# Kernel optimization log

Measured on AMD Instinct MI355X. Metric: run time of the kernel, lower is better.

The kernel has to match this reference:

```python
import jax, jax.numpy as jnp
import numpy as np

TEMPERATURE = 8.0  # sqrt(d_k) with d_k = 64
EPS = 1e-8


def setup_inputs() -> dict:
    key = jax.random.key(0)
    kq, kk, kv, km = jax.random.split(key, 4)
    B, L, D = 16, 2048, 64
    q = jax.random.normal(kq, (B, L, D), dtype=jnp.float32)
    k = jax.random.normal(kk, (B, L, D), dtype=jnp.float32)
    v = jax.random.normal(kv, (B, L, D), dtype=jnp.float32)
    # True entries are zeroed out AFTER softmax (post-softmax masking)
    mask = jax.random.randint(km, (B, L, L), 0, 2).astype(jnp.bool_)
    return {"q": q, "k": k, "v": v, "mask": mask}


def reference(q, k, v, mask):
    # attn scores: [B, Lq, Lk]
    attn = jnp.einsum("bqd,bkd->bqk", q, k) / TEMPERATURE
    attn = jax.nn.softmax(attn, axis=2)
    # post-softmax masking followed by renormalization (breaks flash-attn fusion)
    attn = jnp.where(mask, 0.0, attn)
    attn = attn / (jnp.sum(attn, axis=2, keepdims=True) + EPS)
    # dropout is identity in eval/reference mode
    output = jnp.einsum("bqk,bkd->bqd", attn, v)
    return output, attn
```

## Files before the change

### kernel.cpp

```cpp
#include <hip/hip_runtime.h>

#define BATCH 16
#define LSEQ 2048
#define DIM 64
#define TQ 16
#define SSTRIDE 2056
#define EPSV 1e-8f

typedef float f4 __attribute__((ext_vector_type(4)));
typedef _Float16 h4 __attribute__((ext_vector_type(4)));
typedef _Float16 h8 __attribute__((ext_vector_type(8)));
typedef int i4t __attribute__((ext_vector_type(4)));

__device__ inline h8 cvt_h8(f4 a, f4 b) {
    h8 r;
    r[0] = (_Float16)a[0]; r[1] = (_Float16)a[1];
    r[2] = (_Float16)a[2]; r[3] = (_Float16)a[3];
    r[4] = (_Float16)b[0]; r[5] = (_Float16)b[1];
    r[6] = (_Float16)b[2]; r[7] = (_Float16)b[3];
    return r;
}

__global__ __launch_bounds__(256)
void cvt_k_kernel(const float* __restrict__ k, _Float16* __restrict__ kh) {
    const int idx = blockIdx.x * 256 + threadIdx.x;
    f4 v = ((const f4*)k)[idx];
    h4 h;
    #pragma unroll
    for (int e = 0; e < 4; ++e) h[e] = (_Float16)v[e];
    ((h4*)kh)[idx] = h;
}

__global__ __launch_bounds__(256)
void tr_v_kernel(const float* __restrict__ v, _Float16* __restrict__ vt) {
    __shared__ float tile[64][65];
    const int b = blockIdx.y, k0 = blockIdx.x * 64, t = threadIdx.x;
    const float* vb = v + ((size_t)b * LSEQ + k0) * DIM;
    #pragma unroll
    for (int p = 0; p < 4; ++p) {
        const int row = p * 16 + (t >> 4), c4 = (t & 15) * 4;
        f4 val = *(const f4*)(vb + row * DIM + c4);
        #pragma unroll
        for (int e = 0; e < 4; ++e) tile[row][c4 + e] = val[e];
    }
    __syncthreads();
    _Float16* vtb = vt + (size_t)b * DIM * LSEQ;
    #pragma unroll
    for (int p = 0; p < 4; ++p) {
        const int d = p * 16 + (t >> 4), k4 = (t & 15) * 4;
        h4 h;
        #pragma unroll
        for (int e = 0; e < 4; ++e) h[e] = (_Float16)tile[k4 + e][d];
        *(h4*)(vtb + (size_t)d * LSEQ + k0 + k4) = h;
    }
}

__global__ __launch_bounds__(512, 4)
void attn_kernel(const float* __restrict__ q, const _Float16* __restrict__ kh,
                 const _Float16* __restrict__ vt, const int* __restrict__ mask,
                 float* __restrict__ out, float* __restrict__ attn)
{
    __shared__ __align__(16) _Float16 s_p[TQ][SSTRIDE];
    __shared__ float oacc[8][TQ * 16];
    __shared__ float s_inv[TQ];

    const int b    = blockIdx.y;
    const int q0   = blockIdx.x * TQ;
    const int tid  = threadIdx.x;
    const int w    = tid >> 6;
    const int lane = tid & 63;
    const int quad = lane >> 4;
    const int m16  = lane & 15;

    const float* qrow = q + ((size_t)b * LSEQ + q0 + m16) * DIM + quad * 8;
    h8 aq0 = cvt_h8(*(const f4*)(qrow),      *(const f4*)(qrow + 4));
    h8 aq1 = cvt_h8(*(const f4*)(qrow + 32), *(const f4*)(qrow + 36));

    for (int t = w; t < LSEQ / 16; t += 8) {
        const int c = t * 16;
        const _Float16* krow = kh + ((size_t)b * LSEQ + c + m16) * DIM + quad * 8;
        h8 bk0 = *(const h8*)(krow);
        h8 bk1 = *(const h8*)(krow + 32);
        f4 acc = {0.f, 0.f, 0.f, 0.f};
        acc = __builtin_amdgcn_mfma_f32_16x16x32_f16(aq0, bk0, acc, 0, 0, 0);
        acc = __builtin_amdgcn_mfma_f32_16x16x32_f16(aq1, bk1, acc, 0, 0, 0);
        #pragma unroll
        for (int r = 0; r < 4; ++r)
            s_p[quad * 4 + r][c + m16] = (_Float16)(acc[r] * 0.125f);
    }
    __syncthreads();

    #pragma unroll
    for (int rr = 0; rr < 2; ++rr) {
        const int row = 2 * w + rr;
        const int* mrow = mask + ((size_t)b * LSEQ + q0 + row) * LSEQ;

        i4t mv[8];
        #pragma unroll
        for (int j = 0; j < 8; ++j)
            mv[j] = __builtin_nontemporal_load((const i4t*)(mrow + lane * 4 + 256 * j));

        float sa = 0.f, sk = 0.f;
        h4 pk[8];
        #pragma unroll
        for (int j = 0; j < 8; ++j) {
            h4 hv = *(const h4*)(&s_p[row][lane * 4 + 256 * j]);
            #pragma unroll
            for (int e = 0; e < 4; ++e) {
                float p = __expf((float)hv[e]);
                sa += p;
                float pm = mv[j][e] ? 0.f : p;
                sk += pm;
                pk[j][e] = (_Float16)pm;
            }
        }
        #pragma unroll
        for (int off = 32; off >= 1; off >>= 1) {
            sa += __shfl_xor(sa, off);
            sk += __shfl_xor(sk, off);
        }
        const float inv_d = 1.f / (sk + EPSV * sa);
        if (lane == 0) s_inv[row] = inv_d;

        float* arow = attn + ((size_t)b * LSEQ + q0 + row) * LSEQ;
        #pragma unroll
        for (int j = 0; j < 8; ++j) {
            const int c = lane * 4 + 256 * j;
            *(h4*)(&s_p[row][c]) = pk[j];
            f4 pv;
            #pragma unroll
            for (int e = 0; e < 4; ++e) pv[e] = inv_d * (float)pk[j][e];
            __builtin_nontemporal_store(pv, (f4*)(&arow[c]));
        }
    }
    __syncthreads();

    {
        const int dt = w >> 1;
        const int kh_ = w & 1;
        const _Float16* vtr = vt + ((size_t)b * DIM + dt * 16 + m16) * LSEQ;
        f4 acc = {0.f, 0.f, 0.f, 0.f};
        for (int kb0 = kh_ * 1024; kb0 < kh_ * 1024 + 1024; kb0 += 32) {
            const int kk = kb0 + quad * 8;
            h8 af = *(const h8*)(&s_p[m16][kk]);
            h8 bf = *(const h8*)(vtr + kk);
            acc = __builtin_amdgcn_mfma_f32_16x16x32_f16(af, bf, acc, 0, 0, 0);
        }
        #pragma unroll
        for (int r = 0; r < 4; ++r)
            oacc[w][(quad * 4 + r) * 16 + m16] = acc[r];
    }
    __syncthreads();

    float* ob = out + ((size_t)b * LSEQ + q0) * DIM;
    #pragma unroll
    for (int it = 0; it < 2; ++it) {
        const int idx = tid + it * 512;
        const int row = idx >> 6;
        const int d   = idx & 63;
        const int dt2 = d >> 4, dc = d & 15;
        ob[row * DIM + d] = s_inv[row] *
            (oacc[2 * dt2][row * 16 + dc] + oacc[2 * dt2 + 1][row * 16 + dc]);
    }
}

__global__ __launch_bounds__(512, 4)
void attn_kernel_fb(const float* __restrict__ q, const float* __restrict__ k,
                    const float* __restrict__ v, const int* __restrict__ mask,
                    float* __restrict__ out, float* __restrict__ attn)
{
    __shared__ __align__(16) _Float16 s_p[TQ][SSTRIDE];
    __shared__ float oacc[8][TQ * 16];
    __shared__ float s_inv[TQ];

    const int b = blockIdx.y, q0 = blockIdx.x * TQ, tid = threadIdx.x;
    const int w = tid >> 6, lane = tid & 63, quad = lane >> 4, m16 = lane & 15;
    const float* kp = k + (size_t)b * LSEQ * DIM;
    const float* vp = v + (size_t)b * LSEQ * DIM;
    const float* qrow = q + ((size_t)b * LSEQ + q0 + m16) * DIM + quad * 8;
    h8 aq0 = cvt_h8(*(const f4*)(qrow),      *(const f4*)(qrow + 4));
    h8 aq1 = cvt_h8(*(const f4*)(qrow + 32), *(const f4*)(qrow + 36));

    for (int t = w; t < LSEQ / 16; t += 8) {
        const int c = t * 16;
        const float* krow = kp + (size_t)(c + m16) * DIM + quad * 8;
        h8 bk0 = cvt_h8(*(const f4*)(krow),      *(const f4*)(krow + 4));
        h8 bk1 = cvt_h8(*(const f4*)(krow + 32), *(const f4*)(krow + 36));
        f4 acc = {0.f, 0.f, 0.f, 0.f};
        acc = __builtin_amdgcn_mfma_f32_16x16x32_f16(aq0, bk0, acc, 0, 0, 0);
        acc = __builtin_amdgcn_mfma_f32_16x16x32_f16(aq1, bk1, acc, 0, 0, 0);
        #pragma unroll
        for (int r = 0; r < 4; ++r)
            s_p[quad * 4 + r][c + m16] = (_Float16)(acc[r] * 0.125f);
    }
    __syncthreads();

    #pragma unroll
    for (int rr = 0; rr < 2; ++rr) {
        const int row = 2 * w + rr;
        const int* mrow = mask + ((size_t)b * LSEQ + q0 + row) * LSEQ;
        i4t mv[8];
        #pragma unroll
        for (int j = 0; j < 8; ++j)
            mv[j] = __builtin_nontemporal_load((const i4t*)(mrow + lane * 4 + 256 * j));
        float sa = 0.f, sk = 0.f;
        h4 pk[8];
        #pragma unroll
        for (int j = 0; j < 8; ++j) {
            h4 hv = *(const h4*)(&s_p[row][lane * 4 + 256 * j]);
            #pragma unroll
            for (int e = 0; e < 4; ++e) {
                float p = __expf((float)hv[e]);
                sa += p;
                float pm = mv[j][e] ? 0.f : p;
                sk += pm;
                pk[j][e] = (_Float16)pm;
            }
        }
        #pragma unroll
        for (int off = 32; off >= 1; off >>= 1) {
            sa += __shfl_xor(sa, off);
            sk += __shfl_xor(sk, off);
        }
        const float inv_d = 1.f / (sk + EPSV * sa);
        if (lane == 0) s_inv[row] = inv_d;
        float* arow = attn + ((size_t)b * LSEQ + q0 + row) * LSEQ;
        #pragma unroll
        for (int j = 0; j < 8; ++j) {
            const int c = lane * 4 + 256 * j;
            *(h4*)(&s_p[row][c]) = pk[j];
            f4 pv;
            #pragma unroll
            for (int e = 0; e < 4; ++e) pv[e] = inv_d * (float)pk[j][e];
            __builtin_nontemporal_store(pv, (f4*)(&arow[c]));
        }
    }
    __syncthreads();

    {
        const int dt = w >> 1, kh_ = w & 1;
        f4 acc = {0.f, 0.f, 0.f, 0.f};
        for (int kb0 = kh_ * 1024; kb0 < kh_ * 1024 + 1024; kb0 += 32) {
            const int kk = kb0 + quad * 8;
            h8 af = *(const h8*)(&s_p[m16][kk]);
            const float* vcol = vp + (size_t)kk * DIM + dt * 16 + m16;
            h8 bf;
            #pragma unroll
            for (int j = 0; j < 8; ++j) bf[j] = (_Float16)vcol[j * DIM];
            acc = __builtin_amdgcn_mfma_f32_16x16x32_f16(af, bf, acc, 0, 0, 0);
        }
        #pragma unroll
        for (int r = 0; r < 4; ++r)
            oacc[w][(quad * 4 + r) * 16 + m16] = acc[r];
    }
    __syncthreads();

    float* ob = out + ((size_t)b * LSEQ + q0) * DIM;
    #pragma unroll
    for (int it = 0; it < 2; ++it) {
        const int idx = tid + it * 512;
        const int row = idx >> 6, d = idx & 63;
        const int dt2 = d >> 4, dc = d & 15;
        ob[row * DIM + d] = s_inv[row] *
            (oacc[2 * dt2][row * 16 + dc] + oacc[2 * dt2 + 1][row * 16 + dc]);
    }
}

extern "C" void kernel_launch(void* const* d_in, const int* in_sizes, int n_in,
                              void* d_out, int out_size, void* d_ws, size_t ws_size,
                              hipStream_t stream) {
    const float* q = (const float*)d_in[0];
    const float* k = (const float*)d_in[1];
    const float* v = (const float*)d_in[2];
    const int* mask = (const int*)d_in[3];
    float* out = (float*)d_out;
    float* attn = out + (size_t)BATCH * LSEQ * DIM;
    dim3 grid(LSEQ / TQ, BATCH);

    const size_t kv_elems = (size_t)BATCH * LSEQ * DIM;
    if (ws_size >= kv_elems * 2 * sizeof(_Float16)) {
        _Float16* kh = (_Float16*)d_ws;
        _Float16* vt = kh + kv_elems;
        cvt_k_kernel<<<kv_elems / 4 / 256, 256, 0, stream>>>(k, kh);
        tr_v_kernel<<<dim3(LSEQ / 64, BATCH), 256, 0, stream>>>(v, vt);
        attn_kernel<<<grid, 512, 0, stream>>>(q, kh, vt, mask, out, attn);
    } else {
        attn_kernel_fb<<<grid, 512, 0, stream>>>(q, k, v, mask, out, attn);
    }
}
```

Baseline: 539.7 us.

## Double query tile to 32 rows with 1024-thread blocks and prefetch mask

The attention kernel now processes 32 query rows per block with 16 waves, so each K and V fragment load feeds two MFMAs (rows A and B). This halves K/V global traffic per output. The first mask row is prefetched before the QK^T phase to overlap its latency, and exp is folded into exp2 with a pre-multiplied log2e scale. The cost is double the LDS use for scores (about 130KB per block), which limits occupancy to one block per CU, plus extra syncs in the output reduction.

```diff
diff --git a/kernel.cpp b/kernel.cpp
--- a/kernel.cpp
+++ b/kernel.cpp
@@ -3,9 +3,10 @@
 #define BATCH 16
 #define LSEQ 2048
 #define DIM 64
-#define TQ 16
+#define TQ 32
 #define SSTRIDE 2056
 #define EPSV 1e-8f
+#define SCALE_LOG2E 0.18033688011112042f
 
 typedef float f4 __attribute__((ext_vector_type(4)));
 typedef _Float16 h4 __attribute__((ext_vector_type(4)));
@@ -55,13 +56,13 @@
     }
 }
 
-__global__ __launch_bounds__(512, 4)
+__global__ __launch_bounds__(1024, 4)
 void attn_kernel(const float* __restrict__ q, const _Float16* __restrict__ kh,
                  const _Float16* __restrict__ vt, const int* __restrict__ mask,
                  float* __restrict__ out, float* __restrict__ attn)
 {
     __shared__ __align__(16) _Float16 s_p[TQ][SSTRIDE];
-    __shared__ float oacc[8][TQ * 16];
+    __shared__ float oacc[16][256];
     __shared__ float s_inv[TQ];
 
     const int b    = blockIdx.y;
@@ -72,44 +73,58 @@
     const int quad = lane >> 4;
     const int m16  = lane & 15;
 
-    const float* qrow = q + ((size_t)b * LSEQ + q0 + m16) * DIM + quad * 8;
-    h8 aq0 = cvt_h8(*(const f4*)(qrow),      *(const f4*)(qrow + 4));
-    h8 aq1 = cvt_h8(*(const f4*)(qrow + 32), *(const f4*)(qrow + 36));
-
-    for (int t = w; t < LSEQ / 16; t += 8) {
+    const int row0 = 2 * w;
+    const int* mrow0 = mask + ((size_t)b * LSEQ + q0 + row0) * LSEQ;
+    i4t mv0[8];
+    #pragma unroll
+    for (int j = 0; j < 8; ++j)
+        mv0[j] = __builtin_nontemporal_load((const i4t*)(mrow0 + lane * 4 + 256 * j));
+
+    const float* qrowA = q + ((size_t)b * LSEQ + q0 + m16) * DIM + quad * 8;
+    const float* qrowB = qrowA + 16 * DIM;
+    h8 aqA0 = cvt_h8(*(const f4*)(qrowA),      *(const f4*)(qrowA + 4));
+    h8 aqA1 = cvt_h8(*(const f4*)(qrowA + 32), *(const f4*)(qrowA + 36));
+    h8 aqB0 = cvt_h8(*(const f4*)(qrowB),      *(const f4*)(qrowB + 4));
+    h8 aqB1 = cvt_h8(*(const f4*)(qrowB + 32), *(const f4*)(qrowB + 36));
+
+    for (int t = w; t < LSEQ / 16; t += 16) {
         const int c = t * 16;
         const _Float16* krow = kh + ((size_t)b * LSEQ + c + m16) * DIM + quad * 8;
         h8 bk0 = *(const h8*)(krow);
         h8 bk1 = *(const h8*)(krow + 32);
-        f4 acc = {0.f, 0.f, 0.f, 0.f};
-        acc = __builtin_amdgcn_mfma_f32_16x16x32_f16(aq0, bk0, acc, 0, 0, 0);
-        acc = __builtin_amdgcn_mfma_f32_16x16x32_f16(aq1, bk1, acc, 0, 0, 0);
-        #pragma unroll
-        for (int r = 0; r < 4; ++r)
-            s_p[quad * 4 + r][c + m16] = (_Float16)(acc[r] * 0.125f);
-    }
-    __syncthreads();
+        f4 accA = {0.f, 0.f, 0.f, 0.f}, accB = {0.f, 0.f, 0.f, 0.f};
+        accA = __builtin_amdgcn_mfma_f32_16x16x32_f16(aqA0, bk0, accA, 0, 0, 0);
+        accA = __builtin_amdgcn_mfma_f32_16x16x32_f16(aqA1, bk1, accA, 0, 0, 0);
+        accB = __builtin_amdgcn_mfma_f32_16x16x32_f16(aqB0, bk0, accB, 0, 0, 0);
+        accB = __builtin_amdgcn_mfma_f32_16x16x32_f16(aqB1, bk1, accB, 0, 0, 0);
+        #pragma unroll
+        for (int r = 0; r < 4; ++r) {
+            s_p[quad * 4 + r][c + m16]      = (_Float16)(accA[r] * SCALE_LOG2E);
+            s_p[16 + quad * 4 + r][c + m16] = (_Float16)(accB[r] * SCALE_LOG2E);
+        }
+    }
+    __syncthreads();
+
+    const int* mrow1 = mrow0 + LSEQ;
+    i4t mv1[8];
+    #pragma unroll
+    for (int j = 0; j < 8; ++j)
+        mv1[j] = __builtin_nontemporal_load((const i4t*)(mrow1 + lane * 4 + 256 * j));
 
     #pragma unroll
     for (int rr = 0; rr < 2; ++rr) {
         const int row = 2 * w + rr;
-        const int* mrow = mask + ((size_t)b * LSEQ + q0 + row) * LSEQ;
-
-        i4t mv[8];
-        #pragma unroll
-        for (int j = 0; j < 8; ++j)
-            mv[j] = __builtin_nontemporal_load((const i4t*)(mrow + lane * 4 + 256 * j));
-
         float sa = 0.f, sk = 0.f;
         h4 pk[8];
         #pragma unroll
         for (int j = 0; j < 8; ++j) {
             h4 hv = *(const h4*)(&s_p[row][lane * 4 + 256 * j]);
+            i4t m = rr ? mv1[j] : mv0[j];
             #pragma unroll
             for (int e = 0; e < 4; ++e) {
-                float p = __expf((float)hv[e]);
+                float p = exp2f((float)hv[e]);
                 sa += p;
-                float pm = mv[j][e] ? 0.f : p;
+                float pm = m[e] ? 0.f : p;
                 sk += pm;
                 pk[j][e] = (_Float16)pm;
             }
@@ -135,32 +150,49 @@
     }
     __syncthreads();
 
+    const int dt = w & 3;
+    const int kq = w >> 2;
+    const _Float16* vtr = vt + ((size_t)b * DIM + dt * 16 + m16) * LSEQ;
+    f4 accA = {0.f, 0.f, 0.f, 0.f}, accB = {0.f, 0.f, 0.f, 0.f};
+    #pragma unroll 2
+    for (int kb = kq * 512; kb < kq * 512 + 512; kb += 32) {
+        const int kk = kb + quad * 8;
+        h8 bf  = *(const h8*)(vtr + kk);
+        h8 afA = *(const h8*)(&s_p[m16][kk]);
+        h8 afB = *(const h8*)(&s_p[16 + m16][kk]);
+        accA = __builtin_amdgcn_mfma_f32_16x16x32_f16(afA, bf, accA, 0, 0, 0);
+        accB = __builtin_amdgcn_mfma_f32_16x16x32_f16(afB, bf, accB, 0, 0, 0);
+    }
+
+    float* ob = out + ((size_t)b * LSEQ + q0) * DIM;
+
+    #pragma unroll
+    for (int r = 0; r < 4; ++r)
+        oacc[w][(quad * 4 + r) * 16 + m16] = accA[r];
+    __syncthreads();
     {
-        const int dt = w >> 1;
-        const int kh_ = w & 1;
-        const _Float16* vtr = vt + ((size_t)b * DIM + dt * 16 + m16) * LSEQ;
-        f4 acc = {0.f, 0.f, 0.f, 0.f};
-        for (int kb0 = kh_ * 1024; kb0 < kh_ * 1024 + 1024; kb0 += 32) {
-            const int kk = kb0 + quad * 8;
-            h8 af = *(const h8*)(&s_p[m16][kk]);
-            h8 bf = *(const h8*)(vtr + kk);
-            acc = __builtin_amdgcn_mfma_f32_16x16x32_f16(af, bf, acc, 0, 0, 0);
-        }
-        #pragma unroll
-        for (int r = 0; r < 4; ++r)
-            oacc[w][(quad * 4 + r) * 16 + m16] = acc[r];
-    }
-    __syncthreads();
-
-    float* ob = out + ((size_t)b * LSEQ + q0) * DIM;
-    #pragma unroll
-    for (int it = 0; it < 2; ++it) {
-        const int idx = tid + it * 512;
-        const int row = idx >> 6;
-        const int d   = idx & 63;
+        const int row = tid >> 6;
+        const int d   = tid & 63;
         const int dt2 = d >> 4, dc = d & 15;
-        ob[row * DIM + d] = s_inv[row] *
-            (oacc[2 * dt2][row * 16 + dc] + oacc[2 * dt2 + 1][row * 16 + dc]);
+        const int o   = row * 16 + dc;
+        float vsum = oacc[dt2][o] + oacc[4 + dt2][o]
+                   + oacc[8 + dt2][o] + oacc[12 + dt2][o];
+        ob[row * DIM + d] = s_inv[row] * vsum;
+    }
+    __syncthreads();
+
+    #pragma unroll
+    for (int r = 0; r < 4; ++r)
+        oacc[w][(quad * 4 + r) * 16 + m16] = accB[r];
+    __syncthreads();
+    {
+        const int row = tid >> 6;
+        const int d   = tid & 63;
+        const int dt2 = d >> 4, dc = d & 15;
+        const int o   = row * 16 + dc;
+        float vsum = oacc[dt2][o] + oacc[4 + dt2][o]
+                   + oacc[8 + dt2][o] + oacc[12 + dt2][o];
+        ob[(16 + row) * DIM + d] = s_inv[16 + row] * vsum;
     }
 }
 
@@ -169,11 +201,11 @@
                     const float* __restrict__ v, const int* __restrict__ mask,
                     float* __restrict__ out, float* __restrict__ attn)
 {
-    __shared__ __align__(16) _Float16 s_p[TQ][SSTRIDE];
-    __shared__ float oacc[8][TQ * 16];
-    __shared__ float s_inv[TQ];
-
-    const int b = blockIdx.y, q0 = blockIdx.x * TQ, tid = threadIdx.x;
+    __shared__ __align__(16) _Float16 s_p[16][SSTRIDE];
+    __shared__ float oacc[8][16 * 16];
+    __shared__ float s_inv[16];
+
+    const int b = blockIdx.y, q0 = blockIdx.x * 16, tid = threadIdx.x;
     const int w = tid >> 6, lane = tid & 63, quad = lane >> 4, m16 = lane & 15;
     const float* kp = k + (size_t)b * LSEQ * DIM;
     const float* vp = v + (size_t)b * LSEQ * DIM;
@@ -275,7 +307,6 @@
     const int* mask = (const int*)d_in[3];
     float* out = (float*)d_out;
     float* attn = out + (size_t)BATCH * LSEQ * DIM;
-    dim3 grid(LSEQ / TQ, BATCH);
 
     const size_t kv_elems = (size_t)BATCH * LSEQ * DIM;
     if (ws_size >= kv_elems * 2 * sizeof(_Float16)) {
@@ -283,8 +314,8 @@
         _Float16* vt = kh + kv_elems;
         cvt_k_kernel<<<kv_elems / 4 / 256, 256, 0, stream>>>(k, kh);
         tr_v_kernel<<<dim3(LSEQ / 64, BATCH), 256, 0, stream>>>(v, vt);
-        attn_kernel<<<grid, 512, 0, stream>>>(q, kh, vt, mask, out, attn);
+        attn_kernel<<<dim3(LSEQ / TQ, BATCH), 1024, 0, stream>>>(q, kh, vt, mask, out, attn);
     } else {
-        attn_kernel_fb<<<grid, 512, 0, stream>>>(q, k, v, mask, out, attn);
-    }
-}
+        attn_kernel_fb<<<dim3(LSEQ / 16, BATCH), 512, 0, stream>>>(q, k, v, mask, out, attn);
+    }
+}
```

Measured after the change: 499.7 us. 1.08x faster.
